# Performance work log

Hardware: AMD Instinct MI355X
Metric: run time of the kernel (lower is better)

The kernel has to match this reference:

```python
import jax, jax.numpy as jnp
import numpy as np

NOT_EPSILON = 1.0
W_SCALE = 0.05  # scaled randn init for numerical stability of swishmax logits

H, T, A, C = 8, 1024, 64, 256  # heads, key/query size, attention size, compress size


def swishmax(x, axis):
    m = jnp.max(x, axis=axis, keepdims=True)
    xe = x * jnp.exp(x - m)
    return xe / (jnp.sum(jnp.abs(xe), axis=axis, keepdims=True) + NOT_EPSILON)


def setup_inputs() -> dict:
    key = jax.random.key(0)
    ks = jax.random.split(key, 7)
    B, Q, K = 2, 2048, 2048
    return {
        "query_tokens": jax.random.normal(ks[0], (B, Q, T), dtype=jnp.float32),
        "key_tokens": jax.random.normal(ks[1], (B, K, T), dtype=jnp.float32),
        "key_down": jax.random.normal(ks[2], (H, T, A), dtype=jnp.float32) * W_SCALE,
        "query_down": jax.random.normal(ks[3], (H, T, A), dtype=jnp.float32) * W_SCALE,
        "query_down_bias": jax.random.normal(ks[4], (H, 1, A), dtype=jnp.float32) * W_SCALE,
        "value_down": jax.random.normal(ks[5], (H, T, C), dtype=jnp.float32) * W_SCALE,
        "value_up": jax.random.normal(ks[6], (H, C, T), dtype=jnp.float32) * W_SCALE,
    }


def reference(query_tokens, key_tokens, key_down, query_down, query_down_bias, value_down, value_up):
    # key/query projections: [B,K,T] x [H,T,A] -> [B,H,K,A]
    k = jnp.einsum('bkt,hta->bhka', key_tokens, key_down)
    q = jnp.einsum('bqt,hta->bhqa', query_tokens, query_down) + query_down_bias[None]  # [B,H,Q,A]
    # attention logits: key @ query^T -> [B,H,K,Q]
    logits = jnp.einsum('bhka,bhqa->bhkq', k, q)
    attn = swishmax(logits, axis=-2)  # normalized over keys (dim=-2)
    # sum_k key_tokens[b,k,:] * attn[b,h,k,q]  ==  [B,H,Q,T] (matmul form of the outer-product sum)
    vs = jnp.einsum('bhkq,bkt->bhqt', attn, key_tokens)
    # compress path: value_down then value_up
    vs = jnp.einsum('bhqc,hct->bhqt', jnp.einsum('bhqt,htc->bhqc', vs, value_down), value_up)
    return vs.sum(axis=1)  # sum over heads -> [B,Q,T]
```

## Files before the change

### kernel.cpp

```cpp
#include <hip/hip_runtime.h>
#include <hip/hip_fp16.h>
#include <math.h>


typedef _Float16 f16;
typedef _Float16 f16x4 __attribute__((ext_vector_type(4)));
typedef _Float16 f16x8 __attribute__((ext_vector_type(8)));
typedef short s16x4 __attribute__((ext_vector_type(4)));
typedef short bf16x8 __attribute__((ext_vector_type(8)));
typedef float f32x4 __attribute__((ext_vector_type(4)));

#define MFMA_F16(a, b, c) __builtin_amdgcn_mfma_f32_16x16x32_f16(a, b, c, 0, 0, 0)
#define MFMA_BF16(a, b, c) __builtin_amdgcn_mfma_f32_16x16x32_bf16(a, b, c, 0, 0, 0)

__device__ __forceinline__ void g2lds16(const void* g, void* l) {
  __builtin_amdgcn_global_load_lds((__attribute__((address_space(1))) void*)g,
                                   (__attribute__((address_space(3))) void*)l, 16, 0, 0);
}

__device__ __forceinline__ short f32_bf16(float x) {
  union { float f; unsigned u; } v; v.f = x;
  unsigned r = v.u + 0x7FFFu + ((v.u >> 16) & 1u);
  return (short)(r >> 16);
}
__device__ __forceinline__ float bf16_f32(short h) {
  union { unsigned u; float f; } v; v.u = ((unsigned)(unsigned short)h) << 16;
  return v.f;
}

__global__ __launch_bounds__(256) void ew_split(const float* __restrict__ in,
                                                short* __restrict__ bhi,
                                                short* __restrict__ blo,
                                                f16* __restrict__ fo, int n4) {
  int i = blockIdx.x * 256 + threadIdx.x;
  int stride = gridDim.x * 256;
  for (; i < n4; i += stride) {
    f32x4 v = ((const f32x4*)in)[i];
    s16x4 h, l;
    f16x4 f;
#pragma unroll
    for (int j = 0; j < 4; j++) {
      short hj = f32_bf16(v[j]);
      h[j] = hj;
      l[j] = f32_bf16(v[j] - bf16_f32(hj));
      f[j] = (f16)v[j];
    }
    ((s16x4*)bhi)[i] = h;
    ((s16x4*)blo)[i] = l;
    if (fo) ((f16x4*)fo)[i] = f;
  }
}

__global__ __launch_bounds__(256) void transpose_split(const float* __restrict__ in,
                                                       short* __restrict__ bhi,
                                                       short* __restrict__ blo,
                                                       f16* __restrict__ fo,
                                                       int R, int C) {
  __shared__ float t[64][65];
  int cb = blockIdx.x * 64, rb = blockIdx.y * 64;
  size_t batch = (size_t)blockIdx.z * R * C;
  int tid = threadIdx.x;
#pragma unroll
  for (int i = 0; i < 4; i++) {
    int r = (tid >> 4) + i * 16, c4 = (tid & 15) * 4;
    f32x4 v = *(const f32x4*)(in + batch + (size_t)(rb + r) * C + cb + c4);
    t[r][c4] = v[0]; t[r][c4 + 1] = v[1]; t[r][c4 + 2] = v[2]; t[r][c4 + 3] = v[3];
  }
  __syncthreads();
#pragma unroll
  for (int i = 0; i < 4; i++) {
    int c = (tid >> 4) + i * 16, r4 = (tid & 15) * 4;
    float v0 = t[r4][c], v1 = t[r4 + 1][c], v2 = t[r4 + 2][c], v3 = t[r4 + 3][c];
    size_t o = batch + (size_t)(cb + c) * R + rb + r4;
    if (bhi) {
      s16x4 h = {f32_bf16(v0), f32_bf16(v1), f32_bf16(v2), f32_bf16(v3)};
      *(s16x4*)(bhi + o) = h;
      s16x4 l = {f32_bf16(v0 - bf16_f32(h[0])), f32_bf16(v1 - bf16_f32(h[1])),
                 f32_bf16(v2 - bf16_f32(h[2])), f32_bf16(v3 - bf16_f32(h[3]))};
      *(s16x4*)(blo + o) = l;
    }
    if (fo) {
      f16x4 fv = {(f16)v0, (f16)v1, (f16)v2, (f16)v3};
      *(f16x4*)(fo + o) = fv;
    }
  }
}

__global__ __launch_bounds__(256, 2) void proj_gemm(
    const short* __restrict__ qtok_hi, const short* __restrict__ qtok_lo,
    const short* __restrict__ ktok_hi, const short* __restrict__ ktok_lo,
    const short* __restrict__ wqT_hi, const short* __restrict__ wqT_lo,
    const short* __restrict__ wkT_hi, const short* __restrict__ wkT_lo,
    const float* __restrict__ bias, short* __restrict__ q_split,
    short* __restrict__ k_split) {
  const bool isQ = (blockIdx.z == 0);
  const short* Ahi = isQ ? qtok_hi : ktok_hi;
  const short* Alo = isQ ? qtok_lo : ktok_lo;
  const short* Bhi = isQ ? wqT_hi : wkT_hi;
  const short* Blo = isQ ? wqT_lo : wkT_lo;
  short* outp = isQ ? q_split : k_split;

  __shared__ __attribute__((aligned(16))) short sm[2][4][128 * 32];

  int tid = threadIdx.x, w = tid >> 6, lane = tid & 63, g = lane >> 4, li = lane & 15;
  int mb = blockIdx.y * 128, nb = blockIdx.x * 128;
  int wm = (w >> 1) * 64, wn = (w & 1) * 64;

  f32x4 acc[4][4] = {};

  auto STAGE = [&](int kb, int buf) {
#pragma unroll
    for (int i = 0; i < 2; i++) {
      int off = (w * 2 + i) * 1024 + lane * 16;
      int row = off >> 6;
      int ss = ((off >> 4) & 3) ^ ((row >> 1) & 3);
      size_t asrc = (size_t)(mb + row) * 1024 + kb + ss * 8;
      size_t bsrc = (size_t)(nb + row) * 1024 + kb + ss * 8;
      int dst = (w * 2 + i) * 512;
      g2lds16(Ahi + asrc, &sm[buf][0][dst]);
      g2lds16(Alo + asrc, &sm[buf][1][dst]);
      g2lds16(Bhi + bsrc, &sm[buf][2][dst]);
      g2lds16(Blo + bsrc, &sm[buf][3][dst]);
    }
  };

  STAGE(0, 0);
  __syncthreads();
  for (int kb = 0; kb < 1024; kb += 32) {
    int cur = (kb >> 5) & 1;
    if (kb + 32 < 1024) STAGE(kb + 32, cur ^ 1);
    bf16x8 af[4][2], bf[4][2];
#pragma unroll
    for (int f = 0; f < 4; f++) {
      int ra = wm + f * 16 + li;
      int sa = g ^ ((ra >> 1) & 3);
      af[f][0] = *(const bf16x8*)&sm[cur][0][ra * 32 + sa * 8];
      af[f][1] = *(const bf16x8*)&sm[cur][1][ra * 32 + sa * 8];
      int rb = wn + f * 16 + li;
      int sb = g ^ ((rb >> 1) & 3);
      bf[f][0] = *(const bf16x8*)&sm[cur][2][rb * 32 + sb * 8];
      bf[f][1] = *(const bf16x8*)&sm[cur][3][rb * 32 + sb * 8];
    }
#pragma unroll
    for (int mf = 0; mf < 4; mf++)
#pragma unroll
      for (int nf = 0; nf < 4; nf++) {
        acc[mf][nf] = MFMA_BF16(af[mf][0], bf[nf][0], acc[mf][nf]);
        acc[mf][nf] = MFMA_BF16(af[mf][0], bf[nf][1], acc[mf][nf]);
        acc[mf][nf] = MFMA_BF16(af[mf][1], bf[nf][0], acc[mf][nf]);
      }
    __syncthreads();
  }
#pragma unroll
  for (int mf = 0; mf < 4; mf++)
#pragma unroll
    for (int nf = 0; nf < 4; nf++)
#pragma unroll
      for (int r = 0; r < 4; r++) {
        int m = mb + wm + mf * 16 + 4 * g + r;
        int n = nb + wn + nf * 16 + li;
        float v = acc[mf][nf][r];
        if (isQ) v += bias[n];
        short hi = f32_bf16(v);
        short lo = f32_bf16(v - bf16_f32(hi));
        size_t base = ((size_t)((m >> 11) * 8 + (n >> 6)) * 2048 + (m & 2047)) * 128;
        outp[base + (n & 63)] = hi;
        outp[base + 64 + (n & 63)] = lo;
      }
}

__global__ __launch_bounds__(256, 2) void kv_gemm(const f16* __restrict__ A,
                                                  const f16* __restrict__ Bm,
                                                  f16* __restrict__ kvT) {
  __shared__ __attribute__((aligned(16))) f16 sm[2][2][128 * 32];
  int tid = threadIdx.x, w = tid >> 6, lane = tid & 63, g = lane >> 4, li = lane & 15;
  int mb = blockIdx.y * 128, nb = blockIdx.x * 128;
  int wm = (w >> 1) * 64, wn = (w & 1) * 64;
  f32x4 acc[4][4] = {};

  auto STAGE = [&](int kb, int buf) {
#pragma unroll
    for (int i = 0; i < 2; i++) {
      int off = (w * 2 + i) * 1024 + lane * 16;
      int row = off >> 6;
      int ss = ((off >> 4) & 3) ^ ((row >> 1) & 3);
      int dst = (w * 2 + i) * 512;
      g2lds16(A + (size_t)(mb + row) * 1024 + kb + ss * 8, &sm[buf][0][dst]);
      g2lds16(Bm + (size_t)(nb + row) * 1024 + kb + ss * 8, &sm[buf][1][dst]);
    }
  };

  STAGE(0, 0);
  __syncthreads();
  for (int kb = 0; kb < 1024; kb += 32) {
    int cur = (kb >> 5) & 1;
    if (kb + 32 < 1024) STAGE(kb + 32, cur ^ 1);
    f16x8 af[4], bf[4];
#pragma unroll
    for (int f = 0; f < 4; f++) {
      int ra = wm + f * 16 + li;
      int sa = g ^ ((ra >> 1) & 3);
      af[f] = *(const f16x8*)&sm[cur][0][ra * 32 + sa * 8];
      int rb = wn + f * 16 + li;
      int sb = g ^ ((rb >> 1) & 3);
      bf[f] = *(const f16x8*)&sm[cur][1][rb * 32 + sb * 8];
    }
#pragma unroll
    for (int mf = 0; mf < 4; mf++)
#pragma unroll
      for (int nf = 0; nf < 4; nf++)
        acc[mf][nf] = MFMA_F16(af[mf], bf[nf], acc[mf][nf]);
    __syncthreads();
  }
#pragma unroll
  for (int mf = 0; mf < 4; mf++)
#pragma unroll
    for (int nf = 0; nf < 4; nf++) {
      int m = mb + wm + mf * 16 + 4 * g;
      int n = nb + wn + nf * 16 + li;
      f16x4 v = {(f16)acc[mf][nf][0], (f16)acc[mf][nf][1], (f16)acc[mf][nf][2],
                 (f16)acc[mf][nf][3]};
      size_t o = ((size_t)((m >> 11) * 8 + (n >> 8)) * 256 + (n & 255)) * 2048 + (m & 2047);
      *(f16x4*)(kvT + o) = v;
    }
}

__global__ __launch_bounds__(256, 2) void flash_attn(const short* __restrict__ q_split,
                                                     const short* __restrict__ k_split,
                                                     const f16* __restrict__ kvT,
                                                     f16* __restrict__ vs_c) {
  __shared__ __attribute__((aligned(16))) short k_lds[2][32 * 128];
  __shared__ __attribute__((aligned(16))) f16 kv_lds[2][256 * 32];
  __shared__ __attribute__((aligned(16))) f16 p_lds[4][640];

  const int bid = blockIdx.x;
  const int bh = ((bid & 7) << 1) + ((bid >> 3) & 1);
  const int qb = bid >> 4;
  const int tid = threadIdx.x;
  const int w = tid >> 6, lane = tid & 63, g = lane >> 4, li = lane & 15;

  const short* qrow = q_split + ((size_t)bh * 2048 + qb * 64 + w * 16 + li) * 128;
  bf16x8 qf[2][2];
#pragma unroll
  for (int ach = 0; ach < 2; ach++)
#pragma unroll
    for (int hl = 0; hl < 2; hl++)
      qf[ach][hl] = *(const bf16x8*)(qrow + hl * 64 + ach * 32 + g * 8);

  const short* kbase = k_split + (size_t)bh * 2048 * 128;
  const f16* kvbase = kvT + (size_t)bh * 256 * 2048;

  float m_cur = -INFINITY, m_true = -INFINITY, l_run = 0.f;
  f32x4 acc[16] = {};

  auto STAGE = [&](int kt, int buf) {
#pragma unroll
    for (int i = 0; i < 2; i++) {
      int off = (w * 2 + i) * 1024 + lane * 16;
      int row = off >> 8;
      int ss = ((off >> 4) & 15) ^ (row & 7);
      g2lds16(kbase + (size_t)(kt * 32 + row) * 128 + ss * 8,
              (char*)k_lds[buf] + (w * 2 + i) * 1024);
    }
#pragma unroll
    for (int i = 0; i < 4; i++) {
      int off = (w * 4 + i) * 1024 + lane * 16;
      int c = off >> 6;
      int ss = ((off >> 4) & 3) ^ ((c >> 1) & 3);
      g2lds16(kvbase + (size_t)c * 2048 + kt * 32 + ss * 8,
              (char*)kv_lds[buf] + (w * 4 + i) * 1024);
    }
  };

  STAGE(0, 0);
  __syncthreads();

  for (int kt = 0; kt < 64; kt++) {
    const int cur = kt & 1;
    if (kt < 63) STAGE(kt + 1, cur ^ 1);

    f32x4 s[2] = {};
    __builtin_amdgcn_s_setprio(1);
#pragma unroll
    for (int kc = 0; kc < 2; kc++) {
      const int r = kc * 16 + li;
#pragma unroll
      for (int ach = 0; ach < 2; ach++) {
        int sh = (ach * 4 + g) ^ (r & 7);
        int sl = (8 + ach * 4 + g) ^ (r & 7);
        bf16x8 khi = *(const bf16x8*)((const char*)k_lds[cur] + r * 256 + sh * 16);
        bf16x8 klo = *(const bf16x8*)((const char*)k_lds[cur] + r * 256 + sl * 16);
        s[kc] = MFMA_BF16(khi, qf[ach][0], s[kc]);
        s[kc] = MFMA_BF16(khi, qf[ach][1], s[kc]);
        s[kc] = MFMA_BF16(klo, qf[ach][0], s[kc]);
      }
    }
    __builtin_amdgcn_s_setprio(0);

    float tmax = fmaxf(fmaxf(fmaxf(s[0][0], s[0][1]), fmaxf(s[0][2], s[0][3])),
                       fmaxf(fmaxf(s[1][0], s[1][1]), fmaxf(s[1][2], s[1][3])));
    tmax = fmaxf(tmax, __shfl_xor(tmax, 16));
    tmax = fmaxf(tmax, __shfl_xor(tmax, 32));
    m_true = fmaxf(m_true, tmax);
    if (__any(tmax > m_cur + 4.0f)) {
      float mn = fmaxf(m_cur, tmax);
      float sc = __expf(m_cur - mn);
      l_run *= sc;
#pragma unroll
      for (int i = 0; i < 16; i++) acc[i] *= sc;
      m_cur = mn;
    }
    float ls = 0.f;
    float pv[8];
#pragma unroll
    for (int kc = 0; kc < 2; kc++)
#pragma unroll
      for (int r2 = 0; r2 < 4; r2++) {
        float sv = s[kc][r2];
        float e = sv * __expf(sv - m_cur);
        pv[kc * 4 + r2] = e;
        ls += fabsf(e);
      }
    ls += __shfl_xor(ls, 16);
    ls += __shfl_xor(ls, 32);
    l_run += ls;

#pragma unroll
    for (int kc = 0; kc < 2; kc++) {
      f16x4 p4 = {(f16)pv[kc * 4], (f16)pv[kc * 4 + 1], (f16)pv[kc * 4 + 2],
                  (f16)pv[kc * 4 + 3]};
      *(f16x4*)&p_lds[w][li * 40 + kc * 16 + 4 * g] = p4;
    }
    f16x8 pf = *(const f16x8*)&p_lds[w][li * 40 + 8 * g];

    __builtin_amdgcn_s_setprio(1);
#pragma unroll
    for (int ct = 0; ct < 16; ct++) {
      int c = ct * 16 + li;
      int ss = g ^ ((c >> 1) & 3);
      f16x8 vf = *(const f16x8*)((const char*)kv_lds[cur] + c * 64 + ss * 16);
      acc[ct] = MFMA_F16(vf, pf, acc[ct]);
    }
    __builtin_amdgcn_s_setprio(0);

    __syncthreads();
  }

  float sfix = __expf(m_cur - m_true);
  float invd = sfix / (l_run * sfix + 1.0f);
  f16* orow = vs_c + ((size_t)(bh >> 3) * 2048 + qb * 64 + w * 16 + li) * 2048 + (bh & 7) * 256;
#pragma unroll
  for (int ct = 0; ct < 16; ct++) {
    f16x4 v = {(f16)(acc[ct][0] * invd), (f16)(acc[ct][1] * invd),
               (f16)(acc[ct][2] * invd), (f16)(acc[ct][3] * invd)};
    *(f16x4*)(orow + ct * 16 + 4 * g) = v;
  }
}

__global__ __launch_bounds__(256, 2) void final_gemm(const f16* __restrict__ A,
                                                     const f16* __restrict__ Bm,
                                                     float* __restrict__ outp) {
  __shared__ __attribute__((aligned(16))) f16 sm[2][2][128 * 32];
  int tid = threadIdx.x, w = tid >> 6, lane = tid & 63, g = lane >> 4, li = lane & 15;
  int mb = blockIdx.y * 128, nb = blockIdx.x * 128;
  int wm = (w >> 1) * 64, wn = (w & 1) * 64;
  f32x4 acc[4][4] = {};

  auto STAGE = [&](int kb, int buf) {
#pragma unroll
    for (int i = 0; i < 2; i++) {
      int off = (w * 2 + i) * 1024 + lane * 16;
      int row = off >> 6;
      int ss = ((off >> 4) & 3) ^ ((row >> 1) & 3);
      int dst = (w * 2 + i) * 512;
      g2lds16(A + (size_t)(mb + row) * 2048 + kb + ss * 8, &sm[buf][0][dst]);
      g2lds16(Bm + (size_t)(nb + row) * 2048 + kb + ss * 8, &sm[buf][1][dst]);
    }
  };

  STAGE(0, 0);
  __syncthreads();
  for (int kb = 0; kb < 2048; kb += 32) {
    int cur = (kb >> 5) & 1;
    if (kb + 32 < 2048) STAGE(kb + 32, cur ^ 1);
    f16x8 af[4], bf[4];
#pragma unroll
    for (int f = 0; f < 4; f++) {
      int ra = wm + f * 16 + li;
      int sa = g ^ ((ra >> 1) & 3);
      af[f] = *(const f16x8*)&sm[cur][0][ra * 32 + sa * 8];
      int rb = wn + f * 16 + li;
      int sb = g ^ ((rb >> 1) & 3);
      bf[f] = *(const f16x8*)&sm[cur][1][rb * 32 + sb * 8];
    }
#pragma unroll
    for (int mf = 0; mf < 4; mf++)
#pragma unroll
      for (int nf = 0; nf < 4; nf++)
        acc[mf][nf] = MFMA_F16(af[mf], bf[nf], acc[mf][nf]);
    __syncthreads();
  }
#pragma unroll
  for (int mf = 0; mf < 4; mf++)
#pragma unroll
    for (int nf = 0; nf < 4; nf++)
#pragma unroll
      for (int r = 0; r < 4; r++) {
        int m = mb + wm + mf * 16 + 4 * g + r;
        int n = nb + wn + nf * 16 + li;
        outp[(size_t)m * 1024 + n] = acc[mf][nf][r];
      }
}

extern "C" void kernel_launch(void* const* d_in, const int* in_sizes, int n_in,
                              void* d_out, int out_size, void* d_ws, size_t ws_size,
                              hipStream_t stream) {
  (void)in_sizes; (void)n_in; (void)out_size; (void)ws_size;
  const float* qtok = (const float*)d_in[0];
  const float* ktok = (const float*)d_in[1];
  const float* kdw = (const float*)d_in[2];
  const float* qdw = (const float*)d_in[3];
  const float* qdb = (const float*)d_in[4];
  const float* vdw = (const float*)d_in[5];
  const float* vup = (const float*)d_in[6];

  char* ws = (char*)d_ws;
  size_t off = 0;
  auto take = [&](size_t n) { void* p = ws + off; off += (n + 255) & ~(size_t)255; return p; };

  short* qtok_hi = (short*)take(8u << 20);
  short* qtok_lo = (short*)take(8u << 20);
  short* ktok_hi = (short*)take(8u << 20);
  short* ktok_lo = (short*)take(8u << 20);
  f16* ktok_f = (f16*)take(8u << 20);
  short* wqT_hi = (short*)take(1u << 20);
  short* wqT_lo = (short*)take(1u << 20);
  short* wkT_hi = (short*)take(1u << 20);
  short* wkT_lo = (short*)take(1u << 20);
  f16* vdT = (f16*)take(4u << 20);
  f16* vuT = (f16*)take(4u << 20);
  short* q_split = (short*)take(8u << 20);
  short* k_split = (short*)take(8u << 20);
  f16* kvT = (f16*)(void*)ktok_hi;
  f16* vs_c = (f16*)(void*)qtok_hi;

  ew_split<<<2048, 256, 0, stream>>>(qtok, qtok_hi, qtok_lo, (f16*)nullptr, 1048576);
  ew_split<<<2048, 256, 0, stream>>>(ktok, ktok_hi, ktok_lo, ktok_f, 1048576);
  transpose_split<<<dim3(1, 16, 8), 256, 0, stream>>>(qdw, wqT_hi, wqT_lo, nullptr, 1024, 64);
  transpose_split<<<dim3(1, 16, 8), 256, 0, stream>>>(kdw, wkT_hi, wkT_lo, nullptr, 1024, 64);
  transpose_split<<<dim3(4, 16, 8), 256, 0, stream>>>(vdw, nullptr, nullptr, vdT, 1024, 256);
  transpose_split<<<dim3(16, 32, 1), 256, 0, stream>>>(vup, nullptr, nullptr, vuT, 2048, 1024);

  proj_gemm<<<dim3(4, 32, 2), 256, 0, stream>>>(qtok_hi, qtok_lo, ktok_hi, ktok_lo,
                                                wqT_hi, wqT_lo, wkT_hi, wkT_lo, qdb,
                                                q_split, k_split);
  kv_gemm<<<dim3(16, 32), 256, 0, stream>>>(ktok_f, vdT, kvT);
  flash_attn<<<512, 256, 0, stream>>>(q_split, k_split, kvT, vs_c);
  final_gemm<<<dim3(8, 32), 256, 0, stream>>>(vs_c, vuT, (float*)d_out);
}
```

Before: 228.3 us.

## Restructure flash attention to register-direct loads and halve GEMM M-tiles

The three GEMMs (proj, kv, final) move from 128x128 to 64x128 tiles with twice the grid, and kv_gemm's launch bounds rise so more blocks fit per CU, aiming at better occupancy and CU fill. The kvT layout is reblocked into 32-key chunks so flash_attn can load K and KV fragments straight from global memory into registers, double-buffered in code, with no LDS staging. Each wave now computes a 64-channel slice for all 64 queries, sharing P and the rescale factors through LDS with a barrier per tile. This removes LDS traffic for K/V but adds a cross-wave barrier and relies on global loads hiding their latency.

After: 284.8 us. 1.25x slower.

```diff
diff --git a/kernel.cpp b/kernel.cpp
--- a/kernel.cpp
+++ b/kernel.cpp
@@ -100,27 +100,29 @@
   const short* Blo = isQ ? wqT_lo : wkT_lo;
   short* outp = isQ ? q_split : k_split;
 
-  __shared__ __attribute__((aligned(16))) short sm[2][4][128 * 32];
+  __shared__ __attribute__((aligned(16))) short sm[2][12288];
 
   int tid = threadIdx.x, w = tid >> 6, lane = tid & 63, g = lane >> 4, li = lane & 15;
-  int mb = blockIdx.y * 128, nb = blockIdx.x * 128;
-  int wm = (w >> 1) * 64, wn = (w & 1) * 64;
-
-  f32x4 acc[4][4] = {};
+  int mb = blockIdx.y * 64, nb = blockIdx.x * 128;
+  int wm = (w >> 1) * 32, wn = (w & 1) * 64;
+
+  f32x4 acc[2][4] = {};
 
   auto STAGE = [&](int kb, int buf) {
+    {
+      int off = tid * 16;
+      int row = off >> 6, ss = ((off >> 4) & 3) ^ ((row >> 1) & 3);
+      size_t src = (size_t)(mb + row) * 1024 + kb + ss * 8;
+      g2lds16(Ahi + src, (char*)&sm[buf][0] + w * 1024);
+      g2lds16(Alo + src, (char*)&sm[buf][2048] + w * 1024);
+    }
 #pragma unroll
     for (int i = 0; i < 2; i++) {
-      int off = (w * 2 + i) * 1024 + lane * 16;
-      int row = off >> 6;
-      int ss = ((off >> 4) & 3) ^ ((row >> 1) & 3);
-      size_t asrc = (size_t)(mb + row) * 1024 + kb + ss * 8;
-      size_t bsrc = (size_t)(nb + row) * 1024 + kb + ss * 8;
-      int dst = (w * 2 + i) * 512;
-      g2lds16(Ahi + asrc, &sm[buf][0][dst]);
-      g2lds16(Alo + asrc, &sm[buf][1][dst]);
-      g2lds16(Bhi + bsrc, &sm[buf][2][dst]);
-      g2lds16(Blo + bsrc, &sm[buf][3][dst]);
+      int off = i * 4096 + tid * 16;
+      int row = off >> 6, ss = ((off >> 4) & 3) ^ ((row >> 1) & 3);
+      size_t src = (size_t)(nb + row) * 1024 + kb + ss * 8;
+      g2lds16(Bhi + src, (char*)&sm[buf][4096] + i * 4096 + w * 1024);
+      g2lds16(Blo + src, (char*)&sm[buf][8192] + i * 4096 + w * 1024);
     }
   };
 
@@ -129,20 +131,21 @@
   for (int kb = 0; kb < 1024; kb += 32) {
     int cur = (kb >> 5) & 1;
     if (kb + 32 < 1024) STAGE(kb + 32, cur ^ 1);
-    bf16x8 af[4][2], bf[4][2];
+    bf16x8 af[2][2], bf[4][2];
+#pragma unroll
+    for (int f = 0; f < 2; f++) {
+      int ra = wm + f * 16 + li, sa = g ^ ((ra >> 1) & 3);
+      af[f][0] = *(const bf16x8*)&sm[cur][ra * 32 + sa * 8];
+      af[f][1] = *(const bf16x8*)&sm[cur][2048 + ra * 32 + sa * 8];
+    }
 #pragma unroll
     for (int f = 0; f < 4; f++) {
-      int ra = wm + f * 16 + li;
-      int sa = g ^ ((ra >> 1) & 3);
-      af[f][0] = *(const bf16x8*)&sm[cur][0][ra * 32 + sa * 8];
-      af[f][1] = *(const bf16x8*)&sm[cur][1][ra * 32 + sa * 8];
-      int rb = wn + f * 16 + li;
-      int sb = g ^ ((rb >> 1) & 3);
-      bf[f][0] = *(const bf16x8*)&sm[cur][2][rb * 32 + sb * 8];
-      bf[f][1] = *(const bf16x8*)&sm[cur][3][rb * 32 + sb * 8];
-    }
-#pragma unroll
-    for (int mf = 0; mf < 4; mf++)
+      int rb = wn + f * 16 + li, sb = g ^ ((rb >> 1) & 3);
+      bf[f][0] = *(const bf16x8*)&sm[cur][4096 + rb * 32 + sb * 8];
+      bf[f][1] = *(const bf16x8*)&sm[cur][8192 + rb * 32 + sb * 8];
+    }
+#pragma unroll
+    for (int mf = 0; mf < 2; mf++)
 #pragma unroll
       for (int nf = 0; nf < 4; nf++) {
         acc[mf][nf] = MFMA_BF16(af[mf][0], bf[nf][0], acc[mf][nf]);
@@ -152,7 +155,7 @@
     __syncthreads();
   }
 #pragma unroll
-  for (int mf = 0; mf < 4; mf++)
+  for (int mf = 0; mf < 2; mf++)
 #pragma unroll
     for (int nf = 0; nf < 4; nf++)
 #pragma unroll
@@ -169,24 +172,27 @@
       }
 }
 
-__global__ __launch_bounds__(256, 2) void kv_gemm(const f16* __restrict__ A,
+__global__ __launch_bounds__(256, 4) void kv_gemm(const f16* __restrict__ A,
                                                   const f16* __restrict__ Bm,
                                                   f16* __restrict__ kvT) {
-  __shared__ __attribute__((aligned(16))) f16 sm[2][2][128 * 32];
+  __shared__ __attribute__((aligned(16))) f16 sm[2][6144];
   int tid = threadIdx.x, w = tid >> 6, lane = tid & 63, g = lane >> 4, li = lane & 15;
-  int mb = blockIdx.y * 128, nb = blockIdx.x * 128;
-  int wm = (w >> 1) * 64, wn = (w & 1) * 64;
-  f32x4 acc[4][4] = {};
+  int mb = blockIdx.y * 64, nb = blockIdx.x * 128;
+  int wm = (w >> 1) * 32, wn = (w & 1) * 64;
+  f32x4 acc[2][4] = {};
 
   auto STAGE = [&](int kb, int buf) {
+    {
+      int off = tid * 16;
+      int row = off >> 6, ss = ((off >> 4) & 3) ^ ((row >> 1) & 3);
+      g2lds16(A + (size_t)(mb + row) * 1024 + kb + ss * 8, (char*)&sm[buf][0] + w * 1024);
+    }
 #pragma unroll
     for (int i = 0; i < 2; i++) {
-      int off = (w * 2 + i) * 1024 + lane * 16;
-      int row = off >> 6;
-      int ss = ((off >> 4) & 3) ^ ((row >> 1) & 3);
-      int dst = (w * 2 + i) * 512;
-      g2lds16(A + (size_t)(mb + row) * 1024 + kb + ss * 8, &sm[buf][0][dst]);
-      g2lds16(Bm + (size_t)(nb + row) * 1024 + kb + ss * 8, &sm[buf][1][dst]);
+      int off = i * 4096 + tid * 16;
+      int row = off >> 6, ss = ((off >> 4) & 3) ^ ((row >> 1) & 3);
+      g2lds16(Bm + (size_t)(nb + row) * 1024 + kb + ss * 8,
+              (char*)&sm[buf][2048] + i * 4096 + w * 1024);
     }
   };
 
@@ -195,32 +201,35 @@
   for (int kb = 0; kb < 1024; kb += 32) {
     int cur = (kb >> 5) & 1;
     if (kb + 32 < 1024) STAGE(kb + 32, cur ^ 1);
-    f16x8 af[4], bf[4];
+    f16x8 af[2], bf[4];
+#pragma unroll
+    for (int f = 0; f < 2; f++) {
+      int ra = wm + f * 16 + li, sa = g ^ ((ra >> 1) & 3);
+      af[f] = *(const f16x8*)&sm[cur][ra * 32 + sa * 8];
+    }
 #pragma unroll
     for (int f = 0; f < 4; f++) {
-      int ra = wm + f * 16 + li;
-      int sa = g ^ ((ra >> 1) & 3);
-      af[f] = *(const f16x8*)&sm[cur][0][ra * 32 + sa * 8];
-      int rb = wn + f * 16 + li;
-      int sb = g ^ ((rb >> 1) & 3);
-      bf[f] = *(const f16x8*)&sm[cur][1][rb * 32 + sb * 8];
-    }
-#pragma unroll
-    for (int mf = 0; mf < 4; mf++)
+      int rb = wn + f * 16 + li, sb = g ^ ((rb >> 1) & 3);
+      bf[f] = *(const f16x8*)&sm[cur][2048 + rb * 32 + sb * 8];
+    }
+#pragma unroll
+    for (int mf = 0; mf < 2; mf++)
 #pragma unroll
       for (int nf = 0; nf < 4; nf++)
         acc[mf][nf] = MFMA_F16(af[mf], bf[nf], acc[mf][nf]);
     __syncthreads();
   }
 #pragma unroll
-  for (int mf = 0; mf < 4; mf++)
+  for (int mf = 0; mf < 2; mf++)
 #pragma unroll
     for (int nf = 0; nf < 4; nf++) {
       int m = mb + wm + mf * 16 + 4 * g;
       int n = nb + wn + nf * 16 + li;
       f16x4 v = {(f16)acc[mf][nf][0], (f16)acc[mf][nf][1], (f16)acc[mf][nf][2],
                  (f16)acc[mf][nf][3]};
-      size_t o = ((size_t)((m >> 11) * 8 + (n >> 8)) * 256 + (n & 255)) * 2048 + (m & 2047);
+      int bh = (m >> 11) * 8 + (n >> 8);
+      size_t o = (size_t)bh * 524288 + (size_t)((m & 2047) >> 5) * 8192 +
+                 (size_t)(n & 255) * 32 + (m & 31);
       *(f16x4*)(kvT + o) = v;
     }
 }
@@ -229,9 +238,9 @@
                                                      const short* __restrict__ k_split,
                                                      const f16* __restrict__ kvT,
                                                      f16* __restrict__ vs_c) {
-  __shared__ __attribute__((aligned(16))) short k_lds[2][32 * 128];
-  __shared__ __attribute__((aligned(16))) f16 kv_lds[2][256 * 32];
-  __shared__ __attribute__((aligned(16))) f16 p_lds[4][640];
+  __shared__ __attribute__((aligned(16))) f16 p_lds[2][64 * 64];
+  __shared__ float sc_lds[2][4][16];
+  __shared__ float fix_lds[64];
 
   const int bid = blockIdx.x;
   const int bh = ((bid & 7) << 1) + ((bid >> 3) & 1);
@@ -247,54 +256,42 @@
     for (int hl = 0; hl < 2; hl++)
       qf[ach][hl] = *(const bf16x8*)(qrow + hl * 64 + ach * 32 + g * 8);
 
-  const short* kbase = k_split + (size_t)bh * 2048 * 128;
-  const f16* kvbase = kvT + (size_t)bh * 256 * 2048;
+  const short* kbase = k_split + (size_t)bh * 262144 + li * 128 + g * 8;
+  const f16* kvbase = kvT + (size_t)bh * 524288 + (w * 64 + li) * 32 + g * 8;
 
   float m_cur = -INFINITY, m_true = -INFINITY, l_run = 0.f;
-  f32x4 acc[16] = {};
-
-  auto STAGE = [&](int kt, int buf) {
-#pragma unroll
-    for (int i = 0; i < 2; i++) {
-      int off = (w * 2 + i) * 1024 + lane * 16;
-      int row = off >> 8;
-      int ss = ((off >> 4) & 15) ^ (row & 7);
-      g2lds16(kbase + (size_t)(kt * 32 + row) * 128 + ss * 8,
-              (char*)k_lds[buf] + (w * 2 + i) * 1024);
-    }
-#pragma unroll
-    for (int i = 0; i < 4; i++) {
-      int off = (w * 4 + i) * 1024 + lane * 16;
-      int c = off >> 6;
-      int ss = ((off >> 4) & 3) ^ ((c >> 1) & 3);
-      g2lds16(kvbase + (size_t)c * 2048 + kt * 32 + ss * 8,
-              (char*)kv_lds[buf] + (w * 4 + i) * 1024);
-    }
-  };
-
-  STAGE(0, 0);
-  __syncthreads();
-
-  for (int kt = 0; kt < 64; kt++) {
-    const int cur = kt & 1;
-    if (kt < 63) STAGE(kt + 1, cur ^ 1);
-
+  f32x4 acc[4][4] = {};
+  bf16x8 ka[8], kb2[8];
+  f16x8 kv[4];
+
+#define LOADK(dst, kt)                                                     \
+  do {                                                                     \
+    const short* _p = kbase + (kt) * 4096;                                 \
+    _Pragma("unroll") for (int kc = 0; kc < 2; kc++)                       \
+        _Pragma("unroll") for (int ach = 0; ach < 2; ach++) {              \
+      dst[kc * 4 + ach * 2 + 0] = *(const bf16x8*)(_p + kc * 2048 + ach * 32);      \
+      dst[kc * 4 + ach * 2 + 1] = *(const bf16x8*)(_p + kc * 2048 + 64 + ach * 32); \
+    }                                                                      \
+  } while (0)
+
+#define LOADKV(kt)                                                         \
+  do {                                                                     \
+    const f16* _p = kvbase + (kt) * 8192;                                  \
+    _Pragma("unroll") for (int ct = 0; ct < 4; ct++) kv[ct] =              \
+        *(const f16x8*)(_p + ct * 512);                                    \
+  } while (0)
+
+  auto body = [&](bf16x8* kr, int buf) {
     f32x4 s[2] = {};
     __builtin_amdgcn_s_setprio(1);
 #pragma unroll
-    for (int kc = 0; kc < 2; kc++) {
-      const int r = kc * 16 + li;
+    for (int kc = 0; kc < 2; kc++)
 #pragma unroll
       for (int ach = 0; ach < 2; ach++) {
-        int sh = (ach * 4 + g) ^ (r & 7);
-        int sl = (8 + ach * 4 + g) ^ (r & 7);
-        bf16x8 khi = *(const bf16x8*)((const char*)k_lds[cur] + r * 256 + sh * 16);
-        bf16x8 klo = *(const bf16x8*)((const char*)k_lds[cur] + r * 256 + sl * 16);
-        s[kc] = MFMA_BF16(khi, qf[ach][0], s[kc]);
-        s[kc] = MFMA_BF16(khi, qf[ach][1], s[kc]);
-        s[kc] = MFMA_BF16(klo, qf[ach][0], s[kc]);
-      }
-    }
+        s[kc] = MFMA_BF16(kr[kc * 4 + ach * 2], qf[ach][0], s[kc]);
+        s[kc] = MFMA_BF16(kr[kc * 4 + ach * 2], qf[ach][1], s[kc]);
+        s[kc] = MFMA_BF16(kr[kc * 4 + ach * 2 + 1], qf[ach][0], s[kc]);
+      }
     __builtin_amdgcn_s_setprio(0);
 
     float tmax = fmaxf(fmaxf(fmaxf(s[0][0], s[0][1]), fmaxf(s[0][2], s[0][3])),
@@ -302,14 +299,15 @@
     tmax = fmaxf(tmax, __shfl_xor(tmax, 16));
     tmax = fmaxf(tmax, __shfl_xor(tmax, 32));
     m_true = fmaxf(m_true, tmax);
+    float sc = 1.0f;
     if (__any(tmax > m_cur + 4.0f)) {
       float mn = fmaxf(m_cur, tmax);
-      float sc = __expf(m_cur - mn);
+      sc = __expf(m_cur - mn);
       l_run *= sc;
-#pragma unroll
-      for (int i = 0; i < 16; i++) acc[i] *= sc;
       m_cur = mn;
     }
+    if (g == 0) sc_lds[buf][w][li] = sc;
+
     float ls = 0.f;
     float pv[8];
 #pragma unroll
@@ -329,52 +327,83 @@
     for (int kc = 0; kc < 2; kc++) {
       f16x4 p4 = {(f16)pv[kc * 4], (f16)pv[kc * 4 + 1], (f16)pv[kc * 4 + 2],
                   (f16)pv[kc * 4 + 3]};
-      *(f16x4*)&p_lds[w][li * 40 + kc * 16 + 4 * g] = p4;
-    }
-    f16x8 pf = *(const f16x8*)&p_lds[w][li * 40 + 8 * g];
+      int wb = (((w * 16 + li) * 128 + kc * 32 + g * 8)) ^ ((li & 7) << 4);
+      *(f16x4*)((char*)p_lds[buf] + wb) = p4;
+    }
+    asm volatile("s_waitcnt lgkmcnt(0)\n\ts_barrier" ::: "memory");
+
+#pragma unroll
+    for (int qt = 0; qt < 4; qt++) {
+      float scq = sc_lds[buf][qt][li];
+      if (__any(scq != 1.0f)) {
+#pragma unroll
+        for (int ct = 0; ct < 4; ct++) acc[ct][qt] *= scq;
+      }
+    }
 
     __builtin_amdgcn_s_setprio(1);
 #pragma unroll
-    for (int ct = 0; ct < 16; ct++) {
-      int c = ct * 16 + li;
-      int ss = g ^ ((c >> 1) & 3);
-      f16x8 vf = *(const f16x8*)((const char*)kv_lds[cur] + c * 64 + ss * 16);
-      acc[ct] = MFMA_F16(vf, pf, acc[ct]);
+    for (int qt = 0; qt < 4; qt++) {
+      int rb = (((qt * 16 + li) * 128 + g * 16)) ^ ((li & 7) << 4);
+      f16x8 pf = *(const f16x8*)((const char*)p_lds[buf] + rb);
+#pragma unroll
+      for (int ct = 0; ct < 4; ct++) acc[ct][qt] = MFMA_F16(kv[ct], pf, acc[ct][qt]);
     }
     __builtin_amdgcn_s_setprio(0);
-
-    __syncthreads();
-  }
+  };
+
+  LOADK(ka, 0);
+#pragma unroll 1
+  for (int kt = 0; kt < 64; kt += 2) {
+    LOADKV(kt);
+    LOADK(kb2, kt + 1);
+    body(ka, 0);
+    LOADKV(kt + 1);
+    if (kt + 2 < 64) LOADK(ka, kt + 2);
+    body(kb2, 1);
+  }
+#undef LOADK
+#undef LOADKV
 
   float sfix = __expf(m_cur - m_true);
   float invd = sfix / (l_run * sfix + 1.0f);
-  f16* orow = vs_c + ((size_t)(bh >> 3) * 2048 + qb * 64 + w * 16 + li) * 2048 + (bh & 7) * 256;
-#pragma unroll
-  for (int ct = 0; ct < 16; ct++) {
-    f16x4 v = {(f16)(acc[ct][0] * invd), (f16)(acc[ct][1] * invd),
-               (f16)(acc[ct][2] * invd), (f16)(acc[ct][3] * invd)};
-    *(f16x4*)(orow + ct * 16 + 4 * g) = v;
+  if (g == 0) fix_lds[w * 16 + li] = invd;
+  __syncthreads();
+#pragma unroll
+  for (int qt = 0; qt < 4; qt++) {
+    float iv = fix_lds[qt * 16 + li];
+    f16* orow = vs_c + ((size_t)(bh >> 3) * 2048 + qb * 64 + qt * 16 + li) * 2048 +
+                (bh & 7) * 256 + w * 64 + g * 4;
+#pragma unroll
+    for (int ct = 0; ct < 4; ct++) {
+      f16x4 v = {(f16)(acc[ct][qt][0] * iv), (f16)(acc[ct][qt][1] * iv),
+                 (f16)(acc[ct][qt][2] * iv), (f16)(acc[ct][qt][3] * iv)};
+      *(f16x4*)(orow + ct * 16) = v;
+    }
   }
 }
 
 __global__ __launch_bounds__(256, 2) void final_gemm(const f16* __restrict__ A,
                                                      const f16* __restrict__ Bm,
                                                      float* __restrict__ outp) {
-  __shared__ __attribute__((aligned(16))) f16 sm[2][2][128 * 32];
+  __shared__ __attribute__((aligned(16))) f16 sm[2][6144];
   int tid = threadIdx.x, w = tid >> 6, lane = tid & 63, g = lane >> 4, li = lane & 15;
-  int mb = blockIdx.y * 128, nb = blockIdx.x * 128;
-  int wm = (w >> 1) * 64, wn = (w & 1) * 64;
-  f32x4 acc[4][4] = {};
+  int mb = blockIdx.y * 64, nb = blockIdx.x * 128;
+  int wm = (w >> 1) * 32, wn = (w & 1) * 64;
+  f32x4 acc[2][4] = {};
 
   auto STAGE = [&](int kb, int buf) {
+    {
+      int off = tid * 16;
+      int row = off >> 6, ss = ((off >> 4) & 3) ^ ((row >> 1) & 3);
+      g2lds16(A + (size_t)(mb + row) * 2048 + kb + ss * 8, (char*)&sm[buf][0] + w * 1024);
+    }
 #pragma unroll
     for (int i = 0; i < 2; i++) {
-      int off = (w * 2 + i) * 1024 + lane * 16;
-      int row = off >> 6;
-      int ss = ((off >> 4) & 3) ^ ((row >> 1) & 3);
-      int dst = (w * 2 + i) * 512;
-      g2lds16(A + (size_t)(mb + row) * 2048 + kb + ss * 8, &sm[buf][0][dst]);
-      g2lds16(Bm + (size_t)(nb + row) * 2048 + kb + ss * 8, &sm[buf][1][dst]);
+      int off = i * 4096 + tid * 16;
+      int row = off >> 6, ss = ((off >> 4) & 3) ^ ((row >> 1) & 3);
+      g2lds16(Bm + (size_t)(nb + row) * 2048 + kb + ss * 8,
+              (char*)&sm[buf][2048] + i * 4096 + w * 1024);
     }
   };
 
@@ -383,25 +412,26 @@
   for (int kb = 0; kb < 2048; kb += 32) {
     int cur = (kb >> 5) & 1;
     if (kb + 32 < 2048) STAGE(kb + 32, cur ^ 1);
-    f16x8 af[4], bf[4];
+    f16x8 af[2], bf[4];
+#pragma unroll
+    for (int f = 0; f < 2; f++) {
+      int ra = wm + f * 16 + li, sa = g ^ ((ra >> 1) & 3);
+      af[f] = *(const f16x8*)&sm[cur][ra * 32 + sa * 8];
+    }
 #pragma unroll
     for (int f = 0; f < 4; f++) {
-      int ra = wm + f * 16 + li;
-      int sa = g ^ ((ra >> 1) & 3);
-      af[f] = *(const f16x8*)&sm[cur][0][ra * 32 + sa * 8];
-      int rb = wn + f * 16 + li;
-      int sb = g ^ ((rb >> 1) & 3);
-      bf[f] = *(const f16x8*)&sm[cur][1][rb * 32 + sb * 8];
-    }
-#pragma unroll
-    for (int mf = 0; mf < 4; mf++)
+      int rb = wn + f * 16 + li, sb = g ^ ((rb >> 1) & 3);
+      bf[f] = *(const f16x8*)&sm[cur][2048 + rb * 32 + sb * 8];
+    }
+#pragma unroll
+    for (int mf = 0; mf < 2; mf++)
 #pragma unroll
       for (int nf = 0; nf < 4; nf++)
         acc[mf][nf] = MFMA_F16(af[mf], bf[nf], acc[mf][nf]);
     __syncthreads();
   }
 #pragma unroll
-  for (int mf = 0; mf < 4; mf++)
+  for (int mf = 0; mf < 2; mf++)
 #pragma unroll
     for (int nf = 0; nf < 4; nf++)
 #pragma unroll
@@ -451,10 +481,10 @@
   transpose_split<<<dim3(4, 16, 8), 256, 0, stream>>>(vdw, nullptr, nullptr, vdT, 1024, 256);
   transpose_split<<<dim3(16, 32, 1), 256, 0, stream>>>(vup, nullptr, nullptr, vuT, 2048, 1024);
 
-  proj_gemm<<<dim3(4, 32, 2), 256, 0, stream>>>(qtok_hi, qtok_lo, ktok_hi, ktok_lo,
+  proj_gemm<<<dim3(4, 64, 2), 256, 0, stream>>>(qtok_hi, qtok_lo, ktok_hi, ktok_lo,
                                                 wqT_hi, wqT_lo, wkT_hi, wkT_lo, qdb,
                                                 q_split, k_split);
-  kv_gemm<<<dim3(16, 32), 256, 0, stream>>>(ktok_f, vdT, kvT);
+  kv_gemm<<<dim3(16, 64), 256, 0, stream>>>(ktok_f, vdT, kvT);
   flash_attn<<<512, 256, 0, stream>>>(q_split, k_split, kvT, vs_c);
-  final_gemm<<<dim3(8, 32), 256, 0, stream>>>(vs_c, vuT, (float*)d_out);
-}
+  final_gemm<<<dim3(8, 64), 256, 0, stream>>>(vs_c, vuT, (float*)d_out);
+}
```
